# Kernel tuning notes

Measured on AMD Instinct MI355X. Metric: run time of the kernel, lower is better.

## Reference

```python
import jax, jax.numpy as jnp
import numpy as np

# dims
B, L, HID = 2, 1024, 2048
NH, HD, NKV = 32, 64, 8
INTER = 8192
DSSM, MH, MP, MS, MG, MK = 2048, 32, 64, 64, 1, 4
CONV_DIM = DSSM + 2 * MG * MS
EPS = 1e-5
ROPE_BASE = 1e11
# multipliers from config
KEY_MULT, ATTN_IN, ATTN_OUT = 0.7, 1.2, 0.8
SSM_IN, SSM_OUT = 1.1, 0.9
GATE_MULT, DOWN_MULT = 0.9, 0.8
SSM_MULTS = (1.0, 0.9, 0.8, 1.1, 1.2)


def _rms(x, w, eps=EPS):
    return x * jax.lax.rsqrt(jnp.mean(x * x, -1, keepdims=True) + eps) * w


def _rope(pos, x):  # neox-style, full head_dim; x: (B,L,H,HD)
    half = HD // 2
    inv = ROPE_BASE ** (-jnp.arange(0, HD, 2, dtype=jnp.float32) / HD)
    ang = pos.astype(jnp.float32)[:, None] * inv  # (L, half)
    cos = jnp.cos(ang)[None, :, None, :]
    sin = jnp.sin(ang)[None, :, None, :]
    x1, x2 = x[..., :half], x[..., half:]
    return jnp.concatenate([x1 * cos - x2 * sin, x2 * cos + x1 * sin], -1)


def _mup_vector():
    return jnp.concatenate([
        jnp.full((DSSM,), SSM_MULTS[0], jnp.float32),
        jnp.full((DSSM,), SSM_MULTS[1], jnp.float32),
        jnp.full((MG * MS,), SSM_MULTS[2], jnp.float32),
        jnp.full((MG * MS,), SSM_MULTS[3], jnp.float32),
        jnp.full((MH,), SSM_MULTS[4], jnp.float32),
    ])


def setup_inputs() -> dict:
    key = jax.random.key(0)
    ks = jax.random.split(key, 16)
    s = 0.02
    return {
        "hidden_states": jax.random.normal(ks[0], (B, L, HID), jnp.float32),
        "positions": jnp.arange(L, dtype=jnp.int32),
        "w_in_ln": jnp.ones((HID,), jnp.float32),
        "qkv_w": jax.random.normal(ks[1], (NH * HD + 2 * NKV * HD, HID), jnp.float32) * s,
        "o_w": jax.random.normal(ks[2], (HID, NH * HD), jnp.float32) * s,
        "in_proj_w": jax.random.normal(ks[3], (2 * DSSM + 2 * MG * MS + MH, HID), jnp.float32) * s,
        "conv_w": jax.random.normal(ks[4], (CONV_DIM, MK), jnp.float32) * 0.1,
        "conv_b": jax.random.normal(ks[5], (CONV_DIM,), jnp.float32) * 0.01,
        "A_log": jnp.log(jnp.linspace(1.0, 16.0, MH, dtype=jnp.float32)),
        "dt_bias": jax.random.normal(ks[6], (MH,), jnp.float32) * 0.1,
        "D": jnp.ones((MH,), jnp.float32),
        "ssm_norm_w": jnp.ones((DSSM,), jnp.float32),
        "out_proj_w": jax.random.normal(ks[7], (HID, DSSM), jnp.float32) * s,
        "w_pre_ff_ln": jnp.ones((HID,), jnp.float32),
        "gate_up_w": jax.random.normal(ks[8], (2 * INTER, HID), jnp.float32) * s,
        "down_w": jax.random.normal(ks[9], (HID, INTER), jnp.float32) * s,
    }


def _attention(hs, positions, qkv_w, o_w):
    qkv = hs @ qkv_w.T
    qs, kvs = NH * HD, NKV * HD
    q = qkv[..., :qs].reshape(B, L, NH, HD)
    k = qkv[..., qs:qs + kvs].reshape(B, L, NKV, HD) * KEY_MULT
    v = qkv[..., qs + kvs:].reshape(B, L, NKV, HD)
    q = _rope(positions, q)
    k = _rope(positions, k)
    rep = NH // NKV
    qg = q.reshape(B, L, NKV, rep, HD)
    scores = jnp.einsum('blgrd,bmgd->bgrlm', qg, k) * (HD ** -0.5)
    mask = jnp.tril(jnp.ones((L, L), bool))
    scores = jnp.where(mask[None, None, None], scores, jnp.float32(-1e9))
    attn = jax.nn.softmax(scores, axis=-1)
    out = jnp.einsum('bgrlm,bmgd->blgrd', attn, v).reshape(B, L, NH * HD)
    return out @ o_w.T


def _mamba(hs, in_proj_w, conv_w, conv_b, A_log, dt_bias, D, ssm_norm_w, out_proj_w):
    proj = (hs @ in_proj_w.T) * _mup_vector()  # (B,L,2*DSSM+2*G*S+MH)
    z = proj[..., :DSSM]
    xBC = proj[..., DSSM:DSSM + CONV_DIM]
    dt = proj[..., -MH:]
    # causal depthwise conv1d, kernel MK, then silu
    xpad = jnp.pad(xBC, ((0, 0), (MK - 1, 0), (0, 0)))
    conv = sum(xpad[:, k:k + L, :] * conv_w[:, k] for k in range(MK)) + conv_b
    xBC = jax.nn.silu(conv)
    x = xBC[..., :DSSM].reshape(B, L, MH, MP)
    Bm = xBC[..., DSSM:DSSM + MG * MS].reshape(B, L, MS)  # G=1
    C = xBC[..., DSSM + MG * MS:].reshape(B, L, MS)
    dt = jax.nn.softplus(dt + dt_bias)  # (B,L,MH)
    A = -jnp.exp(A_log)  # (MH,)

    def step(state, inp):  # state: (B,MH,MP,MS)
        x_t, dt_t, b_t, c_t = inp  # (B,MH,MP),(B,MH),(B,MS),(B,MS)
        dA = jnp.exp(dt_t * A)  # (B,MH)
        dBx = dt_t[..., None, None] * x_t[..., None] * b_t[:, None, None, :]
        state = state * dA[..., None, None] + dBx
        y = jnp.einsum('bhps,bs->bhp', state, c_t)
        return state, y

    xs = (jnp.moveaxis(x, 1, 0), jnp.moveaxis(dt, 1, 0),
          jnp.moveaxis(Bm, 1, 0), jnp.moveaxis(C, 1, 0))
    state0 = jnp.zeros((B, MH, MP, MS), hs.dtype)
    _, ys = jax.lax.scan(step, state0, xs)
    y = jnp.moveaxis(ys, 0, 1) + x * D[None, None, :, None]  # (B,L,MH,MP)
    y = y.reshape(B, L, DSSM)
    # gated RMSNorm: gate with silu(z), then rms-normalize
    g = y * jax.nn.silu(z)
    g = _rms(g, ssm_norm_w)
    return g @ out_proj_w.T


def _mlp(x, gate_up_w, down_w):
    gu = x @ gate_up_w.T
    gate = gu[..., :INTER] * GATE_MULT
    up = gu[..., INTER:]
    return (jax.nn.silu(gate) * up) @ down_w.T * DOWN_MULT


def reference(hidden_states, positions, w_in_ln, qkv_w, o_w, in_proj_w, conv_w,
              conv_b, A_log, dt_bias, D, ssm_norm_w, out_proj_w, w_pre_ff_ln,
              gate_up_w, down_w):
    residual = hidden_states
    hs = _rms(hidden_states, w_in_ln)
    attn_h = _attention(hs * ATTN_IN, positions, qkv_w, o_w)
    ssm_h = _mamba(hs * SSM_IN, in_proj_w, conv_w, conv_b, A_log, dt_bias, D,
                   ssm_norm_w, out_proj_w)
    h = attn_h * ATTN_OUT + ssm_h * SSM_OUT + residual
    residual = h
    h = _rms(h, w_pre_ff_ln)
    h = _mlp(h, gate_up_w, down_w)
    return h + residual
```

## Files before the change

### kernel.cpp

```cpp
#include <hip/hip_runtime.h>
#include <hip/hip_bf16.h>
#include <math.h>

#define B_      2
#define L_      1024
#define HID     2048
#define T_      (B_*L_)
#define NH      32
#define HD      64
#define NKV     8
#define INTER   8192
#define DSSM    2048
#define MH      32
#define MP      64
#define MS      64
#define MK      4
#define CONV_DIM 2176
#define QKV_N   3072
#define INPROJ_N 4256
#define CH      16
#define CL      64

typedef __bf16 bf16x8 __attribute__((ext_vector_type(8)));
typedef __bf16 bf16x4 __attribute__((ext_vector_type(4)));
typedef float  floatx4 __attribute__((ext_vector_type(4)));

static const size_t OFF_H2   = 0;
static const size_t OFF_MUP  = 4194304;
static const size_t AR       = 4210688;
static const size_t OFF_WQKV = AR;
static const size_t OFF_WIN  = OFF_WQKV + 3145728;
static const size_t OFF_WO   = OFF_WIN  + 4358144;
static const size_t OFF_WOP  = OFF_WO   + 2097152;
static const size_t OFF_HSB  = OFF_WOP  + 2097152;
static const size_t OFF_HSF  = OFF_HSB  + 2097152;
static const size_t OFF_QKV  = OFF_HSF  + 4194304;
static const size_t OFF_Q    = OFF_QKV  + 6291456;
static const size_t OFF_K    = OFF_Q    + 2097152;
static const size_t OFF_V    = OFF_K    + 524288;
static const size_t OFF_ATT  = OFF_V    + 524288;
static const size_t OFF_PROJ = OFF_ATT  + 2097152;
static const size_t OFF_XBC  = OFF_PROJ + 8716288;
static const size_t OFF_Y    = OFF_XBC  + 4456448;
static const size_t OFF_G    = OFF_Y    + 4194304;
static const size_t OFF_TB   = OFF_QKV;
static const size_t OFF_DEC  = OFF_Q;
static const size_t OFF_LAM  = OFF_V;
static const size_t OFF_HS2B = AR;
static const size_t OFF_GU   = AR + 2097152;
static const size_t OFF_ACTB = OFF_GU + 33554432;
static const size_t OFF_WB2  = OFF_ACTB + 8388608;

__device__ inline float block_sum(float v, float* red) {
#pragma unroll
  for (int o = 32; o > 0; o >>= 1) v += __shfl_down(v, o, 64);
  const int lane = threadIdx.x & 63, wv = threadIdx.x >> 6;
  if (lane == 0) red[wv] = v;
  __syncthreads();
  if (threadIdx.x == 0) red[0] = red[0] + red[1] + red[2] + red[3];
  __syncthreads();
  float r = red[0];
  __syncthreads();
  return r;
}

__device__ inline bf16x8 pack8(float4 a, float4 b, float scale) {
  bf16x8 v;
  v[0] = (__bf16)(a.x * scale); v[1] = (__bf16)(a.y * scale);
  v[2] = (__bf16)(a.z * scale); v[3] = (__bf16)(a.w * scale);
  v[4] = (__bf16)(b.x * scale); v[5] = (__bf16)(b.y * scale);
  v[6] = (__bf16)(b.z * scale); v[7] = (__bf16)(b.w * scale);
  return v;
}

__device__ __forceinline__ void async16(const void* g, void* l) {
  __builtin_amdgcn_global_load_lds(
      (const __attribute__((address_space(1))) void*)g,
      (__attribute__((address_space(3))) void*)l, 16, 0, 0);
}

__global__ __launch_bounds__(256) void cvt_kernel(
    const float* __restrict__ in, __bf16* __restrict__ outp, int n8)
{
  int i = blockIdx.x * 256 + threadIdx.x;
  const int stride = gridDim.x * 256;
  for (; i < n8; i += stride) {
    const float4* p = (const float4*)(in + (size_t)i * 8);
    float4 a = p[0], b = p[1];
    bf16x8 v;
    v[0] = (__bf16)a.x; v[1] = (__bf16)a.y; v[2] = (__bf16)a.z; v[3] = (__bf16)a.w;
    v[4] = (__bf16)b.x; v[5] = (__bf16)b.y; v[6] = (__bf16)b.z; v[7] = (__bf16)b.w;
    *(bf16x8*)(outp + (size_t)i * 8) = v;
  }
}

__global__ __launch_bounds__(256) void copy_kernel(
    const float* __restrict__ in, float* __restrict__ outp)
{
  const size_t i = ((size_t)blockIdx.x * 256 + threadIdx.x) * 4;
  *(float4*)&outp[i] = *(const float4*)&in[i];
}

__global__ __launch_bounds__(256) void gemm_bf_kernel(
    const __bf16* __restrict__ A, const __bf16* __restrict__ W,
    float* __restrict__ out, const float* __restrict__ colscale,
    int N, int K, int ldo, float alpha)
{
  __shared__ __align__(16) __bf16 As[2][128 * 32];
  __shared__ __align__(16) __bf16 Bs[2][128 * 32];
  const int tid = threadIdx.x;
  const int lane = tid & 63, wave = tid >> 6;
  const int fr = lane & 15, fq = lane >> 4;

  const int nwg = (int)(gridDim.x * gridDim.y);
  int lid = (int)(blockIdx.y * gridDim.x + blockIdx.x);
  lid = (lid & 7) * (nwg >> 3) + (lid >> 3);
  const int m0 = (lid & 15) * 128;
  const int n0 = (lid >> 4) * 128;
  const int wm = (wave >> 1) * 64, wn = (wave & 1) * 64;

  const int KS = K / gridDim.z;
  const int kbase = (int)blockIdx.z * KS;

  const int srow = wave * 32 + (lane >> 2);
  const int selem = (lane & 3) * 8;
  const __bf16* ga0 = A + (size_t)(m0 + srow) * K + kbase + selem;
  const __bf16* ga1 = ga0 + (size_t)16 * K;
  int wr0 = n0 + srow;      if (wr0 >= N) wr0 = N - 1;
  int wr1 = n0 + srow + 16; if (wr1 >= N) wr1 = N - 1;
  const __bf16* gb0 = W + (size_t)wr0 * K + kbase + selem;
  const __bf16* gb1 = W + (size_t)wr1 * K + kbase + selem;
  const int sbase = wave * 2 * 512;

  floatx4 acc[4][4];
#pragma unroll
  for (int i = 0; i < 4; i++)
#pragma unroll
    for (int j = 0; j < 4; j++) acc[i][j] = (floatx4){0.f, 0.f, 0.f, 0.f};

  async16(ga0, &As[0][sbase]); async16(ga1, &As[0][sbase + 512]);
  async16(gb0, &Bs[0][sbase]); async16(gb1, &Bs[0][sbase + 512]);
  ga0 += 32; ga1 += 32; gb0 += 32; gb1 += 32;
  __syncthreads();

  const int nsteps = KS >> 5;
  int cur = 0;
  for (int s = 0; s < nsteps; ++s) {
    if (s + 1 < nsteps) {
      async16(ga0, &As[cur ^ 1][sbase]); async16(ga1, &As[cur ^ 1][sbase + 512]);
      async16(gb0, &Bs[cur ^ 1][sbase]); async16(gb1, &Bs[cur ^ 1][sbase + 512]);
      ga0 += 32; ga1 += 32; gb0 += 32; gb1 += 32;
    }
    bf16x8 aF[4], bF[4];
#pragma unroll
    for (int i = 0; i < 4; i++)
      aF[i] = *(const bf16x8*)&As[cur][(wm + i * 16 + fr) * 32 + fq * 8];
#pragma unroll
    for (int j = 0; j < 4; j++)
      bF[j] = *(const bf16x8*)&Bs[cur][(wn + j * 16 + fr) * 32 + fq * 8];
#pragma unroll
    for (int i = 0; i < 4; i++)
#pragma unroll
      for (int j = 0; j < 4; j++)
        acc[i][j] = __builtin_amdgcn_mfma_f32_16x16x32_bf16(aF[i], bF[j], acc[i][j], 0, 0, 0);
    __syncthreads();
    cur ^= 1;
  }

  const bool at = (gridDim.z > 1);
#pragma unroll
  for (int i = 0; i < 4; i++) {
#pragma unroll
    for (int r = 0; r < 4; r++) {
      const int m = m0 + wm + i * 16 + fq * 4 + r;
      float* orow = out + (size_t)m * ldo;
#pragma unroll
      for (int j = 0; j < 4; j++) {
        const int n = n0 + wn + j * 16 + fr;
        if (n < N) {
          float vv = acc[i][j][r] * alpha;
          if (colscale) vv *= colscale[n];
          if (at) atomicAdd(&orow[n], vv);
          else    orow[n] = vv;
        }
      }
    }
  }
}

__global__ __launch_bounds__(512, 2) void gemm256_kernel(
    const __bf16* __restrict__ A, const __bf16* __restrict__ W,
    float* __restrict__ out, int N, int K, int ldo, float alpha)
{
  __shared__ __align__(16) __bf16 As[2][256 * 64];
  __shared__ __align__(16) __bf16 Bs[2][256 * 64];
  const int tid = threadIdx.x;
  const int lane = tid & 63, wave = tid >> 6;
  const int fr = lane & 15, fq = lane >> 4;

  const int nwg = (int)(gridDim.x * gridDim.y);
  int lid = (int)(blockIdx.y * gridDim.x + blockIdx.x);
  lid = (lid & 7) * (nwg >> 3) + (lid >> 3);
  const int m0 = (lid & 7) * 256;
  const int n0 = (lid >> 3) * 256;
  const int wm = (wave >> 2) * 128;
  const int wn = (wave & 3) * 64;

  const int KS = K / gridDim.z;
  const int kbase = (int)blockIdx.z * KS;

  const int strow = wave * 8 + (lane >> 3);
  const int stcol = (lane & 7) * 8;
  const __bf16* gA = A + (size_t)(m0 + strow) * K + kbase + stcol;
  const __bf16* gB[4];
#pragma unroll
  for (int q = 0; q < 4; q++) {
    int nr = n0 + q * 64 + strow;
    if (nr >= N) nr = N - 1;
    gB[q] = W + (size_t)nr * K + kbase + stcol;
  }
  const int sdst = wave * 512;

  floatx4 acc[8][4];
#pragma unroll
  for (int i = 0; i < 8; i++)
#pragma unroll
    for (int j = 0; j < 4; j++) acc[i][j] = (floatx4){0.f, 0.f, 0.f, 0.f};

#pragma unroll
  for (int q = 0; q < 4; q++) {
    async16(gA + (size_t)q * 64 * K, &As[0][q * 4096 + sdst]);
    async16(gB[q],                   &Bs[0][q * 4096 + sdst]);
  }
  __syncthreads();

  const int nsteps = KS >> 6;
  int cur = 0;
  for (int s = 0; s < nsteps; ++s) {
    if (s + 1 < nsteps) {
      const int ko = (s + 1) * 64;
#pragma unroll
      for (int q = 0; q < 4; q++) {
        async16(gA + ko + (size_t)q * 64 * K, &As[cur ^ 1][q * 4096 + sdst]);
        async16(gB[q] + ko,                   &Bs[cur ^ 1][q * 4096 + sdst]);
      }
    }

    bf16x8 bF[4][2];
#pragma unroll
    for (int j = 0; j < 4; j++)
#pragma unroll
      for (int t = 0; t < 2; t++)
        bF[j][t] = *(const bf16x8*)&Bs[cur][(wn + j * 16 + fr) * 64 + t * 32 + fq * 8];
#pragma unroll
    for (int i = 0; i < 8; i++) {
      bf16x8 a0 = *(const bf16x8*)&As[cur][(wm + i * 16 + fr) * 64 + fq * 8];
      bf16x8 a1 = *(const bf16x8*)&As[cur][(wm + i * 16 + fr) * 64 + 32 + fq * 8];
#pragma unroll
      for (int j = 0; j < 4; j++) {
        acc[i][j] = __builtin_amdgcn_mfma_f32_16x16x32_bf16(a0, bF[j][0], acc[i][j], 0, 0, 0);
        acc[i][j] = __builtin_amdgcn_mfma_f32_16x16x32_bf16(a1, bF[j][1], acc[i][j], 0, 0, 0);
      }
    }
    __syncthreads();
    cur ^= 1;
  }

  const bool at = (gridDim.z > 1);
#pragma unroll
  for (int i = 0; i < 8; i++) {
#pragma unroll
    for (int r = 0; r < 4; r++) {
      const int m = m0 + wm + i * 16 + fq * 4 + r;
      float* orow = out + (size_t)m * ldo;
#pragma unroll
      for (int j = 0; j < 4; j++) {
        const int n = n0 + wn + j * 16 + fr;
        if (n < N) {
          float vv = acc[i][j][r] * alpha;
          if (at) atomicAdd(&orow[n], vv);
          else    orow[n] = vv;
        }
      }
    }
  }
}

__global__ __launch_bounds__(256) void rms_kernel(
    const float* __restrict__ in, const float* __restrict__ w,
    __bf16* __restrict__ outb, float* __restrict__ outf, float* __restrict__ copy)
{
  __shared__ float buf[HID];
  __shared__ float red[8];
  const int tid = threadIdx.x;
  const size_t t = blockIdx.x;
  const float* row = in + t * HID;
  float ss = 0.f;
  for (int i = tid; i < HID; i += 256) { float x = row[i]; buf[i] = x; ss += x * x; }
  float tot = block_sum(ss, red);
  float inv = rsqrtf(tot / (float)HID + 1e-5f);
  for (int i = tid; i < HID; i += 256) {
    float x = buf[i];
    float val = x * inv * w[i];
    outb[t * HID + i] = (__bf16)val;
    if (outf) outf[t * HID + i] = val;
    if (copy) copy[t * HID + i] = x;
  }
}

__global__ void mup_kernel(float* __restrict__ mup) {
  int i = blockIdx.x * 256 + threadIdx.x;
  if (i >= INPROJ_N) return;
  float v = (i < DSSM) ? 1.0f
          : (i < 2 * DSSM) ? 0.9f
          : (i < 2 * DSSM + MS) ? 0.8f
          : (i < 2 * DSSM + 2 * MS) ? 1.1f
          : 1.2f;
  mup[i] = v;
}

__global__ __launch_bounds__(256) void rope_kernel(
    const float* __restrict__ qkv, const int* __restrict__ positions,
    __bf16* __restrict__ q, __bf16* __restrict__ k, __bf16* __restrict__ v)
{
  __shared__ float inv_s[32];
  const int tid = threadIdx.x;
  const size_t t = blockIdx.x;
  const int l = (int)(t & (L_ - 1));
  if (tid < 32) inv_s[tid] = powf(1.0e11f, -(float)(2 * tid) / 64.f);
  __syncthreads();
  const float pos = (float)positions[l];
  const float* src = qkv + t * QKV_N;
  for (int idx = tid; idx < 1536; idx += 256) {
    int head = idx >> 5, hd = idx & 31;
    if (head < 32) {
      float ang = pos * inv_s[hd];
      float c = cosf(ang), sn = sinf(ang);
      float x1 = src[head * 64 + hd], x2 = src[head * 64 + 32 + hd];
      __bf16* dst = q + (t * NH + head) * HD;
      dst[hd] = (__bf16)((x1 * c - x2 * sn) * 0.125f);
      dst[hd + 32] = (__bf16)((x2 * c + x1 * sn) * 0.125f);
    } else if (head < 40) {
      int kk = head - 32;
      float ang = pos * inv_s[hd];
      float c = cosf(ang), sn = sinf(ang);
      float x1 = src[2048 + kk * 64 + hd] * 0.7f;
      float x2 = src[2048 + kk * 64 + 32 + hd] * 0.7f;
      __bf16* dst = k + (t * NKV + kk) * HD;
      dst[hd] = (__bf16)(x1 * c - x2 * sn);
      dst[hd + 32] = (__bf16)(x2 * c + x1 * sn);
    } else {
      int vv = head - 40;
      __bf16* dst = v + (t * NKV + vv) * HD;
      dst[hd] = (__bf16)src[2560 + vv * 64 + hd];
      dst[hd + 32] = (__bf16)src[2560 + vv * 64 + 32 + hd];
    }
  }
}

__global__ __launch_bounds__(256) void fattn_kernel(
    const __bf16* __restrict__ q, const __bf16* __restrict__ k,
    const __bf16* __restrict__ v, __bf16* __restrict__ out)
{
  __shared__ __align__(16) __bf16 Vt[64][72];
  __shared__ __align__(16) __bf16 Ps[4][16][72];
  const int tid = threadIdx.x;
  const int wave = tid >> 6, lane = tid & 63;
  const int fr = lane & 15, fq = lane >> 4;
  const int qt = (int)(gridDim.x - 1) - blockIdx.x;
  const int h = blockIdx.y, b = blockIdx.z, g = h >> 2;
  const int l0 = qt * 64;

  bf16x8 qf[2];
  {
    const int qrow = l0 + wave * 16 + fr;
    const __bf16* qp = q + (((size_t)(b * L_ + qrow)) * NH + h) * HD;
    qf[0] = *(const bf16x8*)&qp[fq * 8];
    qf[1] = *(const bf16x8*)&qp[32 + fq * 8];
  }

  floatx4 O[4];
  float m_run[4], l_run[4];
#pragma unroll
  for (int i = 0; i < 4; i++) { O[i] = (floatx4){0.f,0.f,0.f,0.f}; m_run[i] = -3.0e38f; l_run[i] = 0.f; }

  for (int kt = 0; kt <= qt; kt++) {
    __syncthreads();
#pragma unroll
    for (int pp = 0; pp < 4; pp++) {
      const int kb = pp * 4 + wave;
      bf16x4 pk;
#pragma unroll
      for (int c = 0; c < 4; c++)
        pk[c] = v[(((size_t)(b * L_ + kt * 64 + kb * 4 + c)) * NKV + g) * HD + lane];
      *(bf16x4*)&Vt[lane][kb * 4] = pk;
    }

    floatx4 S[4];
#pragma unroll
    for (int j = 0; j < 4; j++) {
      const __bf16* kp = k + (((size_t)(b * L_ + kt * 64 + j * 16 + fr)) * NKV + g) * HD;
      floatx4 sa = (floatx4){0.f,0.f,0.f,0.f};
#pragma unroll
      for (int s = 0; s < 2; s++) {
        bf16x8 kf = *(const bf16x8*)&kp[s * 32 + fq * 8];
        sa = __builtin_amdgcn_mfma_f32_16x16x32_bf16(qf[s], kf, sa, 0, 0, 0);
      }
      S[j] = sa;
    }

    if (kt == qt) {
      const int qbase = wave * 16 + fq * 4;
#pragma unroll
      for (int j = 0; j < 4; j++)
#pragma unroll
        for (int r = 0; r < 4; r++)
          if (j * 16 + fr > qbase + r) S[j][r] = -1.0e30f;
    }

    float rm[4], alpha[4], rsum[4];
#pragma unroll
    for (int r = 0; r < 4; r++)
      rm[r] = fmaxf(fmaxf(S[0][r], S[1][r]), fmaxf(S[2][r], S[3][r]));
#pragma unroll
    for (int msk = 1; msk <= 8; msk <<= 1)
#pragma unroll
      for (int r = 0; r < 4; r++) rm[r] = fmaxf(rm[r], __shfl_xor(rm[r], msk, 64));
#pragma unroll
    for (int r = 0; r < 4; r++) {
      float mnew = fmaxf(m_run[r], rm[r]);
      alpha[r] = __expf(m_run[r] - mnew);
      m_run[r] = mnew;
    }
#pragma unroll
    for (int j = 0; j < 4; j++)
#pragma unroll
      for (int r = 0; r < 4; r++) S[j][r] = __expf(S[j][r] - m_run[r]);
#pragma unroll
    for (int r = 0; r < 4; r++)
      rsum[r] = S[0][r] + S[1][r] + S[2][r] + S[3][r];
#pragma unroll
    for (int msk = 1; msk <= 8; msk <<= 1)
#pragma unroll
      for (int r = 0; r < 4; r++) rsum[r] += __shfl_xor(rsum[r], msk, 64);
#pragma unroll
    for (int r = 0; r < 4; r++) l_run[r] = l_run[r] * alpha[r] + rsum[r];
#pragma unroll
    for (int d4 = 0; d4 < 4; d4++)
#pragma unroll
      for (int r = 0; r < 4; r++) O[d4][r] *= alpha[r];

#pragma unroll
    for (int j = 0; j < 4; j++)
#pragma unroll
      for (int r = 0; r < 4; r++)
        Ps[wave][fq * 4 + r][j * 16 + fr] = (__bf16)S[j][r];

    __syncthreads();

#pragma unroll
    for (int s = 0; s < 2; s++) {
      bf16x8 pf = *(const bf16x8*)&Ps[wave][fr][s * 32 + fq * 8];
#pragma unroll
      for (int d4 = 0; d4 < 4; d4++) {
        bf16x8 vf = *(const bf16x8*)&Vt[d4 * 16 + fr][s * 32 + fq * 8];
        O[d4] = __builtin_amdgcn_mfma_f32_16x16x32_bf16(pf, vf, O[d4], 0, 0, 0);
      }
    }
  }

  float rl[4];
#pragma unroll
  for (int r = 0; r < 4; r++) rl[r] = 1.f / l_run[r];
#pragma unroll
  for (int d4 = 0; d4 < 4; d4++)
#pragma unroll
    for (int r = 0; r < 4; r++) {
      const int qg = l0 + wave * 16 + fq * 4 + r;
      out[((size_t)(b * L_ + qg)) * HID + h * 64 + d4 * 16 + fr] = (__bf16)(O[d4][r] * rl[r]);
    }
}

__global__ __launch_bounds__(256) void dtfix_kernel(
    const float* __restrict__ hs_ln, const float* __restrict__ w, float* __restrict__ proj)
{
  const size_t t = blockIdx.x;
  const int tid = threadIdx.x;
  const int o = tid >> 3, part = tid & 7;
  const float* a = hs_ln + t * HID;
  const float* wr = w + (size_t)(INPROJ_N - MH + o) * HID;
  float s = 0.f;
  for (int kk = part * 4; kk < HID; kk += 32) {
    const float4 av = *(const float4*)&a[kk];
    const float4 wv = *(const float4*)&wr[kk];
    s += av.x * wv.x + av.y * wv.y + av.z * wv.z + av.w * wv.w;
  }
  s += __shfl_xor(s, 1);
  s += __shfl_xor(s, 2);
  s += __shfl_xor(s, 4);
  if (part == 0) proj[t * INPROJ_N + (INPROJ_N - MH) + o] = s * 1.32f;
}

__global__ __launch_bounds__(256) void conv_kernel(
    const float* __restrict__ proj, const float* __restrict__ cw,
    const float* __restrict__ cb, float* __restrict__ xbc)
{
  const int c = blockIdx.x * 256 + threadIdx.x;
  if (c >= CONV_DIM) return;
  const int t = blockIdx.y;
  const int l = t & (L_ - 1);
  float acc = cb[c];
#pragma unroll
  for (int kk = 0; kk < MK; kk++) {
    int lp = l - (MK - 1) + kk;
    if (lp >= 0)
      acc += proj[((size_t)(t - (MK - 1) + kk)) * INPROJ_N + DSSM + c] * cw[c * MK + kk];
  }
  xbc[(size_t)t * CONV_DIM + c] = acc / (1.f + __expf(-acc));
}

__global__ __launch_bounds__(256) void scanA_kernel(
    const float* __restrict__ xbc, const float* __restrict__ proj,
    const float* __restrict__ A_log, const float* __restrict__ dt_bias,
    const float* __restrict__ Dp,
    float* __restrict__ y, float* __restrict__ Tbuf,
    float* __restrict__ lam, float* __restrict__ dec)
{
  __shared__ __align__(16) __bf16 xT[64][72];
  __shared__ __align__(16) __bf16 BTw[64][72];
  __shared__ __align__(16) __bf16 Braw[64][72];
  __shared__ __align__(16) __bf16 Craw[64][72];
  __shared__ __align__(16) __bf16 Ps[4][16][72];
  __shared__ float dt_s[64], cum_s[64];

  const int tid = threadIdx.x;
  const int lane = tid & 63, wave = tid >> 6;
  const int fr = lane & 15, fq = lane >> 4;
  const int c = blockIdx.x, h = blockIdx.y, b = blockIdx.z;
  const int t0 = b * L_ + c * CL;
  const float Ah = -expf(A_log[h]);
  const float dtb = dt_bias[h], Dh = Dp[h];

  if (wave == 0) {
    float draw = proj[(size_t)(t0 + lane) * INPROJ_N + (INPROJ_N - MH) + h];
    float dtv = draw + dtb;
    dtv = (dtv > 20.f) ? dtv : log1pf(__expf(dtv));
    float cs = dtv * Ah;
#pragma unroll
    for (int d = 1; d < 64; d <<= 1) {
      float nv = __shfl_up(cs, d, 64);
      if (lane >= d) cs += nv;
    }
    dt_s[lane] = dtv;
    cum_s[lane] = cs;
  }

#pragma unroll
  for (int pass = 0; pass < 4; pass++) {
    const int l = pass * 16 + (tid >> 4);
    const int s4 = (tid & 15) * 4;
    const float* rowp = xbc + (size_t)(t0 + l) * CONV_DIM;
    float4 xv = *(const float4*)&rowp[h * 64 + s4];
    float4 bv = *(const float4*)&rowp[DSSM + s4];
    float4 cv = *(const float4*)&rowp[DSSM + MS + s4];
    xT[s4 + 0][l] = (__bf16)xv.x;
    xT[s4 + 1][l] = (__bf16)xv.y;
    xT[s4 + 2][l] = (__bf16)xv.z;
    xT[s4 + 3][l] = (__bf16)xv.w;
    bf16x4 b4; b4[0]=(__bf16)bv.x; b4[1]=(__bf16)bv.y; b4[2]=(__bf16)bv.z; b4[3]=(__bf16)bv.w;
    *(bf16x4*)&Braw[l][s4] = b4;
    bf16x4 c4; c4[0]=(__bf16)cv.x; c4[1]=(__bf16)cv.y; c4[2]=(__bf16)cv.z; c4[3]=(__bf16)cv.w;
    *(bf16x4*)&Craw[l][s4] = c4;
  }
  __syncthreads();

  const float cend = cum_s[63];
#pragma unroll
  for (int pass = 0; pass < 4; pass++) {
    const int l = pass * 16 + (tid >> 4);
    const int s4 = (tid & 15) * 4;
    const float wl = __expf(cend - cum_s[l]) * dt_s[l];
    float4 bv = *(const float4*)&xbc[(size_t)(t0 + l) * CONV_DIM + DSSM + s4];
    BTw[s4 + 0][l] = (__bf16)(bv.x * wl);
    BTw[s4 + 1][l] = (__bf16)(bv.y * wl);
    BTw[s4 + 2][l] = (__bf16)(bv.z * wl);
    BTw[s4 + 3][l] = (__bf16)(bv.w * wl);
  }

  {
    bf16x8 aF0 = *(const bf16x8*)&Craw[wave * 16 + fr][fq * 8];
    bf16x8 aF1 = *(const bf16x8*)&Craw[wave * 16 + fr][fq * 8 + 32];
#pragma unroll
    for (int j = 0; j < 4; j++) {
      floatx4 s = (floatx4){0.f,0.f,0.f,0.f};
      bf16x8 b0 = *(const bf16x8*)&Braw[j * 16 + fr][fq * 8];
      bf16x8 b1 = *(const bf16x8*)&Braw[j * 16 + fr][fq * 8 + 32];
      s = __builtin_amdgcn_mfma_f32_16x16x32_bf16(aF0, b0, s, 0, 0, 0);
      s = __builtin_amdgcn_mfma_f32_16x16x32_bf16(aF1, b1, s, 0, 0, 0);
      const int m = j * 16 + fr;
      const float dtm = dt_s[m], cmm = cum_s[m];
#pragma unroll
      for (int r = 0; r < 4; r++) {
        const int lR = wave * 16 + fq * 4 + r;
        float f = (m <= lR) ? __expf(cum_s[lR] - cmm) * dtm : 0.f;
        Ps[wave][fq * 4 + r][m] = (__bf16)(s[r] * f);
      }
    }
  }
  __syncthreads();

  {
    bf16x8 aF0 = *(const bf16x8*)&Ps[wave][fr][fq * 8];
    bf16x8 aF1 = *(const bf16x8*)&Ps[wave][fr][fq * 8 + 32];
#pragma unroll
    for (int j = 0; j < 4; j++) {
      floatx4 s = (floatx4){0.f,0.f,0.f,0.f};
      bf16x8 b0 = *(const bf16x8*)&xT[j * 16 + fr][fq * 8];
      bf16x8 b1 = *(const bf16x8*)&xT[j * 16 + fr][fq * 8 + 32];
      s = __builtin_amdgcn_mfma_f32_16x16x32_bf16(aF0, b0, s, 0, 0, 0);
      s = __builtin_amdgcn_mfma_f32_16x16x32_bf16(aF1, b1, s, 0, 0, 0);
      const int p = j * 16 + fr;
#pragma unroll
      for (int r = 0; r < 4; r++) {
        const int lR = wave * 16 + fq * 4 + r;
        float xval = (float)xT[p][lR];
        y[(size_t)(t0 + lR) * DSSM + h * 64 + p] = s[r] + Dh * xval;
      }
    }
  }

  {
    float* Tb = Tbuf + ((size_t)((b * MH + h) * CH + c)) * 4096;
    bf16x8 aF0 = *(const bf16x8*)&xT[wave * 16 + fr][fq * 8];
    bf16x8 aF1 = *(const bf16x8*)&xT[wave * 16 + fr][fq * 8 + 32];
#pragma unroll
    for (int j = 0; j < 4; j++) {
      floatx4 s = (floatx4){0.f,0.f,0.f,0.f};
      bf16x8 b0 = *(const bf16x8*)&BTw[j * 16 + fr][fq * 8];
      bf16x8 b1 = *(const bf16x8*)&BTw[j * 16 + fr][fq * 8 + 32];
      s = __builtin_amdgcn_mfma_f32_16x16x32_bf16(aF0, b0, s, 0, 0, 0);
      s = __builtin_amdgcn_mfma_f32_16x16x32_bf16(aF1, b1, s, 0, 0, 0);
#pragma unroll
      for (int r = 0; r < 4; r++)
        Tb[(wave * 16 + fq * 4 + r) * 64 + j * 16 + fr] = s[r];
    }
  }

  if (tid == 0) lam[(b * MH + h) * CH + c] = __expf(cend);
  if (tid >= 64 && tid < 128)
    dec[((size_t)((b * MH + h) * CH + c)) * 64 + (tid - 64)] = __expf(cum_s[tid - 64]);
}

__global__ __launch_bounds__(256) void scanB_kernel(
    const float* __restrict__ xbc, const float* __restrict__ Tbuf,
    const float* __restrict__ lam, const float* __restrict__ dec,
    float* __restrict__ y)
{
  __shared__ __align__(16) float S[64][68];
  __shared__ __align__(16) __bf16 Cc[64][72];
  __shared__ float decl[64];
  const int tid = threadIdx.x;
  const int lane = tid & 63, wave = tid >> 6;
  const int fr = lane & 15, fq = lane >> 4;
  const int h = blockIdx.x, b = blockIdx.y;

  const int sown = tid & 63, pbase = (tid >> 6) * 16;
#pragma unroll
  for (int i = 0; i < 16; i++) S[pbase + i][sown] = 0.f;
  __syncthreads();

  for (int c = 0; c < CH; c++) {
    const int t0 = b * L_ + c * CL;
#pragma unroll
    for (int pass = 0; pass < 4; pass++) {
      const int l = pass * 16 + (tid >> 4);
      const int s4 = (tid & 15) * 4;
      float4 cv = *(const float4*)&xbc[(size_t)(t0 + l) * CONV_DIM + DSSM + MS + s4];
      bf16x4 c4; c4[0]=(__bf16)cv.x; c4[1]=(__bf16)cv.y; c4[2]=(__bf16)cv.z; c4[3]=(__bf16)cv.w;
      *(bf16x4*)&Cc[l][s4] = c4;
    }
    if (tid < 64) decl[tid] = dec[((size_t)((b * MH + h) * CH + c)) * 64 + tid];
    __syncthreads();

    if (c > 0) {
      bf16x8 aF0 = *(const bf16x8*)&Cc[wave * 16 + fr][fq * 8];
      bf16x8 aF1 = *(const bf16x8*)&Cc[wave * 16 + fr][fq * 8 + 32];
#pragma unroll
      for (int j = 0; j < 4; j++) {
        const float* srow = &S[j * 16 + fr][0];
        float4 s0 = *(const float4*)&srow[fq * 8];
        float4 s1 = *(const float4*)&srow[fq * 8 + 4];
        float4 s2 = *(const float4*)&srow[fq * 8 + 32];
        float4 s3 = *(const float4*)&srow[fq * 8 + 36];
        bf16x8 b0 = pack8(s0, s1, 1.f);
        bf16x8 b1 = pack8(s2, s3, 1.f);
        floatx4 acc = (floatx4){0.f,0.f,0.f,0.f};
        acc = __builtin_amdgcn_mfma_f32_16x16x32_bf16(aF0, b0, acc, 0, 0, 0);
        acc = __builtin_amdgcn_mfma_f32_16x16x32_bf16(aF1, b1, acc, 0, 0, 0);
        const int p = j * 16 + fr;
#pragma unroll
        for (int r = 0; r < 4; r++) {
          const int lR = wave * 16 + fq * 4 + r;
          float* yp = &y[(size_t)(t0 + lR) * DSSM + h * 64 + p];
          *yp += decl[lR] * acc[r];
        }
      }
    }
    __syncthreads();

    const float lc = lam[(b * MH + h) * CH + c];
    const float* Tb = Tbuf + ((size_t)((b * MH + h) * CH + c)) * 4096;
#pragma unroll
    for (int i = 0; i < 16; i++) {
      float tv = Tb[(pbase + i) * 64 + sown];
      S[pbase + i][sown] = lc * S[pbase + i][sown] + tv;
    }
    __syncthreads();
  }
}

__global__ __launch_bounds__(256) void gating_kernel(
    const float* __restrict__ y, const float* __restrict__ proj,
    const float* __restrict__ nw, __bf16* __restrict__ g)
{
  __shared__ float buf[DSSM];
  __shared__ float red[8];
  const int tid = threadIdx.x;
  const size_t t = blockIdx.x;
  float ss = 0.f;
  for (int i = tid; i < DSSM; i += 256) {
    float zv = proj[t * INPROJ_N + i];
    float yv = y[t * DSSM + i];
    float gv = yv * zv / (1.f + __expf(-zv));
    buf[i] = gv;
    ss += gv * gv;
  }
  float tot = block_sum(ss, red);
  float inv = rsqrtf(tot / (float)DSSM + 1e-5f);
  for (int i = tid; i < DSSM; i += 256) g[t * DSSM + i] = (__bf16)(buf[i] * inv * nw[i]);
}

__global__ __launch_bounds__(256) void act_kernel(
    const float* __restrict__ gu, __bf16* __restrict__ act)
{
  const int i = (blockIdx.x * 256 + threadIdx.x) * 4;
  const size_t t = blockIdx.y;
  float4 g4 = *(const float4*)&gu[t * (2 * INTER) + i];
  float4 u4 = *(const float4*)&gu[t * (2 * INTER) + INTER + i];
  bf16x4 o;
  float gt;
  gt = g4.x * 0.9f; o[0] = (__bf16)(gt / (1.f + __expf(-gt)) * u4.x);
  gt = g4.y * 0.9f; o[1] = (__bf16)(gt / (1.f + __expf(-gt)) * u4.y);
  gt = g4.z * 0.9f; o[2] = (__bf16)(gt / (1.f + __expf(-gt)) * u4.z);
  gt = g4.w * 0.9f; o[3] = (__bf16)(gt / (1.f + __expf(-gt)) * u4.w);
  *(bf16x4*)&act[t * INTER + i] = o;
}

extern "C" void kernel_launch(void* const* d_in, const int* in_sizes, int n_in,
                              void* d_out, int out_size, void* d_ws, size_t ws_size,
                              hipStream_t stream)
{
  const float* hidden      = (const float*)d_in[0];
  const int*   positions   = (const int*)d_in[1];
  const float* w_in_ln     = (const float*)d_in[2];
  const float* qkv_w       = (const float*)d_in[3];
  const float* o_w         = (const float*)d_in[4];
  const float* in_proj_w   = (const float*)d_in[5];
  const float* conv_w      = (const float*)d_in[6];
  const float* conv_b      = (const float*)d_in[7];
  const float* A_log       = (const float*)d_in[8];
  const float* dt_bias     = (const float*)d_in[9];
  const float* Dp          = (const float*)d_in[10];
  const float* ssm_norm_w  = (const float*)d_in[11];
  const float* out_proj_w  = (const float*)d_in[12];
  const float* w_pre_ff_ln = (const float*)d_in[13];
  const float* gate_up_w   = (const float*)d_in[14];
  const float* down_w      = (const float*)d_in[15];
  (void)in_sizes; (void)n_in; (void)out_size; (void)ws_size;

  float* ws   = (float*)d_ws;
  float* outp = (float*)d_out;

  float*  h2    = ws + OFF_H2;
  float*  mup   = ws + OFF_MUP;
  __bf16* wqkv  = (__bf16*)(ws + OFF_WQKV);
  __bf16* win   = (__bf16*)(ws + OFF_WIN);
  __bf16* wo    = (__bf16*)(ws + OFF_WO);
  __bf16* wop   = (__bf16*)(ws + OFF_WOP);
  __bf16* hsb   = (__bf16*)(ws + OFF_HSB);
  float*  hsf   = ws + OFF_HSF;
  float*  qkv   = ws + OFF_QKV;
  __bf16* qb    = (__bf16*)(ws + OFF_Q);
  __bf16* kb    = (__bf16*)(ws + OFF_K);
  __bf16* vb    = (__bf16*)(ws + OFF_V);
  __bf16* attb  = (__bf16*)(ws + OFF_ATT);
  float*  proj  = ws + OFF_PROJ;
  float*  xbc   = ws + OFF_XBC;
  float*  y     = ws + OFF_Y;
  __bf16* gb    = (__bf16*)(ws + OFF_G);
  float*  Tbuf  = ws + OFF_TB;
  float*  dec   = ws + OFF_DEC;
  float*  lam   = ws + OFF_LAM;
  __bf16* hs2b  = (__bf16*)(ws + OFF_HS2B);
  float*  gu    = ws + OFF_GU;
  __bf16* actb  = (__bf16*)(ws + OFF_ACTB);
  __bf16* wb2   = (__bf16*)(ws + OFF_WB2);

  cvt_kernel<<<2048, 256, 0, stream>>>(qkv_w, wqkv, 786432);
  cvt_kernel<<<2048, 256, 0, stream>>>(in_proj_w, win, 1089536);
  cvt_kernel<<<2048, 256, 0, stream>>>(o_w, wo, 524288);
  cvt_kernel<<<2048, 256, 0, stream>>>(out_proj_w, wop, 524288);
  mup_kernel<<<17, 256, 0, stream>>>(mup);
  rms_kernel<<<T_, 256, 0, stream>>>(hidden, w_in_ln, hsb, hsf, h2);

  gemm_bf_kernel<<<dim3(16, 24, 1), 256, 0, stream>>>(hsb, wqkv, qkv, nullptr,
                                                      QKV_N, HID, QKV_N, 1.2f);
  rope_kernel<<<T_, 256, 0, stream>>>(qkv, positions, qb, kb, vb);
  fattn_kernel<<<dim3(L_ / 64, NH, B_), 256, 0, stream>>>(qb, kb, vb, attb);
  gemm256_kernel<<<dim3(8, 8, 4), 512, 0, stream>>>(attb, wo, h2,
                                                    HID, HID, HID, 0.8f);

  gemm_bf_kernel<<<dim3(16, 34, 1), 256, 0, stream>>>(hsb, win, proj, mup,
                                                      INPROJ_N, HID, INPROJ_N, 1.1f);
  dtfix_kernel<<<T_, 256, 0, stream>>>(hsf, in_proj_w, proj);
  conv_kernel<<<dim3(9, T_), 256, 0, stream>>>(proj, conv_w, conv_b, xbc);
  scanA_kernel<<<dim3(CH, MH, B_), 256, 0, stream>>>(xbc, proj, A_log, dt_bias, Dp,
                                                     y, Tbuf, lam, dec);
  scanB_kernel<<<dim3(MH, B_), 256, 0, stream>>>(xbc, Tbuf, lam, dec, y);
  gating_kernel<<<T_, 256, 0, stream>>>(y, proj, ssm_norm_w, gb);
  gemm256_kernel<<<dim3(8, 8, 4), 512, 0, stream>>>(gb, wop, h2,
                                                    HID, HID, HID, 0.9f);

  rms_kernel<<<T_, 256, 0, stream>>>(h2, w_pre_ff_ln, hs2b, nullptr, nullptr);
  cvt_kernel<<<2048, 256, 0, stream>>>(gate_up_w, wb2, 2097152);
  gemm256_kernel<<<dim3(8, 32, 1), 512, 0, stream>>>(hs2b, wb2, gu,
                                                     INTER, HID, 2 * INTER, 1.0f);
  cvt_kernel<<<2048, 256, 0, stream>>>(gate_up_w + (size_t)INTER * HID, wb2, 2097152);
  gemm256_kernel<<<dim3(8, 32, 1), 512, 0, stream>>>(hs2b, wb2, gu + INTER,
                                                     INTER, HID, 2 * INTER, 1.0f);
  act_kernel<<<dim3(INTER / 1024, T_), 256, 0, stream>>>(gu, actb);
  cvt_kernel<<<2048, 256, 0, stream>>>(down_w, wb2, 2097152);
  copy_kernel<<<4096, 256, 0, stream>>>(h2, outp);
  gemm256_kernel<<<dim3(8, 8, 4), 512, 0, stream>>>(actb, wb2, outp,
                                                    HID, INTER, HID, 0.8f);
}
```

Baseline: 1.191 ms.

## Swizzle LDS layout and pipeline waits in 256-tile bf16 GEMM

Rewrites the 256x256 MFMA GEMM so global-to-LDS staging uses an XOR-swizzled column layout, which removes LDS bank conflicts on fragment reads. The per-iteration __syncthreads is replaced by explicit vmcnt/lgkmcnt waits and raw barriers, so the next tile's loads can stay in flight while the current tile is computed. All A and B fragments for each k-half are loaded before the MFMA burst, which runs under raised wave priority. The N-bounds clamp and check are dropped, which is only safe because every call uses N as a multiple of 256.

Measured after the change: 1.166 ms. -2.1%, faster.

```diff
diff --git a/kernel.cpp b/kernel.cpp
--- a/kernel.cpp
+++ b/kernel.cpp
@@ -188,7 +188,7 @@
   }
 }
 
-__global__ __launch_bounds__(512, 2) void gemm256_kernel(
+__global__ __launch_bounds__(512, 2) void gemm256p_kernel(
     const __bf16* __restrict__ A, const __bf16* __restrict__ W,
     float* __restrict__ out, int N, int K, int ldo, float alpha)
 {
@@ -203,84 +203,88 @@
   lid = (lid & 7) * (nwg >> 3) + (lid >> 3);
   const int m0 = (lid & 7) * 256;
   const int n0 = (lid >> 3) * 256;
-  const int wm = (wave >> 2) * 128;
-  const int wn = (wave & 3) * 64;
+  const int wmL = (wave >> 2) * 128;
+  const int wnL = (wave & 3) * 64;
 
   const int KS = K / gridDim.z;
   const int kbase = (int)blockIdx.z * KS;
 
-  const int strow = wave * 8 + (lane >> 3);
-  const int stcol = (lane & 7) * 8;
-  const __bf16* gA = A + (size_t)(m0 + strow) * K + kbase + stcol;
-  const __bf16* gB[4];
+  const int rwl = wave * 8 + (lane >> 3);
+  const int csw = (((lane & 7) ^ ((lane >> 3) & 7))) * 8;
+  const __bf16* gAq[4];
+  const __bf16* gBq[4];
 #pragma unroll
   for (int q = 0; q < 4; q++) {
-    int nr = n0 + q * 64 + strow;
-    if (nr >= N) nr = N - 1;
-    gB[q] = W + (size_t)nr * K + kbase + stcol;
+    gAq[q] = A + (size_t)(m0 + q * 64 + rwl) * K + kbase + csw;
+    gBq[q] = W + (size_t)(n0 + q * 64 + rwl) * K + kbase + csw;
   }
   const int sdst = wave * 512;
 
+#define STAGE256(buf, ko)                                        \
+  do {                                                           \
+    _Pragma("unroll")                                            \
+    for (int q = 0; q < 4; q++) {                                \
+      async16(gAq[q] + (ko), &As[buf][q * 4096 + sdst]);         \
+      async16(gBq[q] + (ko), &Bs[buf][q * 4096 + sdst]);         \
+    }                                                            \
+  } while (0)
+
   floatx4 acc[8][4];
 #pragma unroll
   for (int i = 0; i < 8; i++)
 #pragma unroll
     for (int j = 0; j < 4; j++) acc[i][j] = (floatx4){0.f, 0.f, 0.f, 0.f};
 
-#pragma unroll
-  for (int q = 0; q < 4; q++) {
-    async16(gA + (size_t)q * 64 * K, &As[0][q * 4096 + sdst]);
-    async16(gB[q],                   &Bs[0][q * 4096 + sdst]);
-  }
-  __syncthreads();
-
-  const int nsteps = KS >> 6;
-  int cur = 0;
-  for (int s = 0; s < nsteps; ++s) {
-    if (s + 1 < nsteps) {
-      const int ko = (s + 1) * 64;
-#pragma unroll
-      for (int q = 0; q < 4; q++) {
-        async16(gA + ko + (size_t)q * 64 * K, &As[cur ^ 1][q * 4096 + sdst]);
-        async16(gB[q] + ko,                   &Bs[cur ^ 1][q * 4096 + sdst]);
-      }
-    }
-
-    bf16x8 bF[4][2];
-#pragma unroll
-    for (int j = 0; j < 4; j++)
-#pragma unroll
-      for (int t = 0; t < 2; t++)
-        bF[j][t] = *(const bf16x8*)&Bs[cur][(wn + j * 16 + fr) * 64 + t * 32 + fq * 8];
-#pragma unroll
-    for (int i = 0; i < 8; i++) {
-      bf16x8 a0 = *(const bf16x8*)&As[cur][(wm + i * 16 + fr) * 64 + fq * 8];
-      bf16x8 a1 = *(const bf16x8*)&As[cur][(wm + i * 16 + fr) * 64 + 32 + fq * 8];
+  STAGE256(0, 0);
+
+  const int ns = KS >> 6;
+  for (int kt = 0; kt < ns; ++kt) {
+    const int c = kt & 1;
+    if (kt + 1 < ns) {
+      STAGE256(c ^ 1, (kt + 1) * 64);
+      asm volatile("s_waitcnt vmcnt(8)" ::: "memory");
+    } else {
+      asm volatile("s_waitcnt vmcnt(0)" ::: "memory");
+    }
+    __builtin_amdgcn_s_barrier();
+
+#pragma unroll
+    for (int kh = 0; kh < 2; ++kh) {
+      const int sw = ((kh * 4 + fq) ^ (fr & 7)) * 8;
+      bf16x8 aF[8], bF[4];
+#pragma unroll
+      for (int j = 0; j < 4; j++)
+        bF[j] = *(const bf16x8*)&Bs[c][(wnL + j * 16 + fr) * 64 + sw];
+#pragma unroll
+      for (int i = 0; i < 8; i++)
+        aF[i] = *(const bf16x8*)&As[c][(wmL + i * 16 + fr) * 64 + sw];
+      asm volatile("s_waitcnt lgkmcnt(0)" ::: "memory");
+      __builtin_amdgcn_sched_barrier(0);
+      __builtin_amdgcn_s_setprio(1);
+#pragma unroll
+      for (int i = 0; i < 8; i++)
+#pragma unroll
+        for (int j = 0; j < 4; j++)
+          acc[i][j] = __builtin_amdgcn_mfma_f32_16x16x32_bf16(aF[i], bF[j], acc[i][j], 0, 0, 0);
+      __builtin_amdgcn_s_setprio(0);
+    }
+    __builtin_amdgcn_s_barrier();
+  }
+#undef STAGE256
+
+  const bool at = (gridDim.z > 1);
+#pragma unroll
+  for (int i = 0; i < 8; i++) {
+#pragma unroll
+    for (int r = 0; r < 4; r++) {
+      const int m = m0 + wmL + i * 16 + fq * 4 + r;
+      float* orow = out + (size_t)m * ldo;
 #pragma unroll
       for (int j = 0; j < 4; j++) {
-        acc[i][j] = __builtin_amdgcn_mfma_f32_16x16x32_bf16(a0, bF[j][0], acc[i][j], 0, 0, 0);
-        acc[i][j] = __builtin_amdgcn_mfma_f32_16x16x32_bf16(a1, bF[j][1], acc[i][j], 0, 0, 0);
-      }
-    }
-    __syncthreads();
-    cur ^= 1;
-  }
-
-  const bool at = (gridDim.z > 1);
-#pragma unroll
-  for (int i = 0; i < 8; i++) {
-#pragma unroll
-    for (int r = 0; r < 4; r++) {
-      const int m = m0 + wm + i * 16 + fq * 4 + r;
-      float* orow = out + (size_t)m * ldo;
-#pragma unroll
-      for (int j = 0; j < 4; j++) {
-        const int n = n0 + wn + j * 16 + fr;
-        if (n < N) {
-          float vv = acc[i][j][r] * alpha;
-          if (at) atomicAdd(&orow[n], vv);
-          else    orow[n] = vv;
-        }
+        const int n = n0 + wnL + j * 16 + fr;
+        float vv = acc[i][j][r] * alpha;
+        if (at) atomicAdd(&orow[n], vv);
+        else    orow[n] = vv;
       }
     }
   }
@@ -817,8 +821,8 @@
                                                       QKV_N, HID, QKV_N, 1.2f);
   rope_kernel<<<T_, 256, 0, stream>>>(qkv, positions, qb, kb, vb);
   fattn_kernel<<<dim3(L_ / 64, NH, B_), 256, 0, stream>>>(qb, kb, vb, attb);
-  gemm256_kernel<<<dim3(8, 8, 4), 512, 0, stream>>>(attb, wo, h2,
-                                                    HID, HID, HID, 0.8f);
+  gemm256p_kernel<<<dim3(8, 8, 4), 512, 0, stream>>>(attb, wo, h2,
+                                                     HID, HID, HID, 0.8f);
 
   gemm_bf_kernel<<<dim3(16, 34, 1), 256, 0, stream>>>(hsb, win, proj, mup,
                                                       INPROJ_N, HID, INPROJ_N, 1.1f);
@@ -828,19 +832,19 @@
                                                      y, Tbuf, lam, dec);
   scanB_kernel<<<dim3(MH, B_), 256, 0, stream>>>(xbc, Tbuf, lam, dec, y);
   gating_kernel<<<T_, 256, 0, stream>>>(y, proj, ssm_norm_w, gb);
-  gemm256_kernel<<<dim3(8, 8, 4), 512, 0, stream>>>(gb, wop, h2,
-                                                    HID, HID, HID, 0.9f);
+  gemm256p_kernel<<<dim3(8, 8, 4), 512, 0, stream>>>(gb, wop, h2,
+                                                     HID, HID, HID, 0.9f);
 
   rms_kernel<<<T_, 256, 0, stream>>>(h2, w_pre_ff_ln, hs2b, nullptr, nullptr);
   cvt_kernel<<<2048, 256, 0, stream>>>(gate_up_w, wb2, 2097152);
-  gemm256_kernel<<<dim3(8, 32, 1), 512, 0, stream>>>(hs2b, wb2, gu,
-                                                     INTER, HID, 2 * INTER, 1.0f);
+  gemm256p_kernel<<<dim3(8, 32, 1), 512, 0, stream>>>(hs2b, wb2, gu,
+                                                      INTER, HID, 2 * INTER, 1.0f);
   cvt_kernel<<<2048, 256, 0, stream>>>(gate_up_w + (size_t)INTER * HID, wb2, 2097152);
-  gemm256_kernel<<<dim3(8, 32, 1), 512, 0, stream>>>(hs2b, wb2, gu + INTER,
-                                                     INTER, HID, 2 * INTER, 1.0f);
+  gemm256p_kernel<<<dim3(8, 32, 1), 512, 0, stream>>>(hs2b, wb2, gu + INTER,
+                                                      INTER, HID, 2 * INTER, 1.0f);
   act_kernel<<<dim3(INTER / 1024, T_), 256, 0, stream>>>(gu, actb);
   cvt_kernel<<<2048, 256, 0, stream>>>(down_w, wb2, 2097152);
   copy_kernel<<<4096, 256, 0, stream>>>(h2, outp);
-  gemm256_kernel<<<dim3(8, 8, 4), 512, 0, stream>>>(actb, wb2, outp,
-                                                    HID, INTER, HID, 0.8f);
-}
+  gemm256p_kernel<<<dim3(8, 8, 4), 512, 0, stream>>>(actb, wb2, outp,
+                                                     HID, INTER, HID, 0.8f);
+}
```
